# Performance work log

Measured on AMD Instinct MI355X. Metric: run time of the kernel, lower is better.

The kernel has to match this reference:

```python
import jax, jax.numpy as jnp
import numpy as np

VOCAB = 4101
NUM_IGNORED = 5  # token ids {0,1,2,3,4} are ignored


def _calc_frequency(x):
    # x: [N, L] int token ids -> [N, VOCAB] scaled frequency vectors
    n = x.shape[0]
    hist = jnp.zeros((n, VOCAB), dtype=jnp.float32)
    hist = hist.at[jnp.arange(n)[:, None], x].add(1.0)  # batched bincount
    hist = hist.at[:, :NUM_IGNORED].set(0.0)            # drop ignored tokens
    seq_len = hist.sum(axis=-1, keepdims=True)          # count of kept tokens
    return jnp.where(seq_len > 0, hist / seq_len * 10.0, hist)


def _mlp(h, W1, b1, W2, b2):
    h = jax.nn.relu(h @ W1 + b1)
    return h @ W2 + b2


def setup_inputs() -> dict:
    key = jax.random.key(0)
    k1, k2, k3 = jax.random.split(key, 3)
    B, L = 1024, 4096
    X = jax.random.randint(k1, (B, 3, L), 0, VOCAB, dtype=jnp.int64)
    W1 = jax.random.normal(k2, (VOCAB, 768), dtype=jnp.float32) * 0.02
    b1 = jnp.zeros((768,), dtype=jnp.float32)
    W2 = jax.random.normal(k3, (768, 256), dtype=jnp.float32) * 0.02
    b2 = jnp.zeros((256,), dtype=jnp.float32)
    return {"X": X, "W1": W1, "b1": b1, "W2": W2, "b2": b2}


def reference(X, W1, b1, W2, b2):
    B, three, L = X.shape
    flat = X.reshape(B * three, L)          # process anchor/pos/neg together
    freq = _calc_frequency(flat)            # [3B, VOCAB]
    out = _mlp(freq, W1, b1, W2, b2)        # [3B, 256]
    out = out.reshape(B, three, 256)
    return (out[:, 0], out[:, 1], out[:, 2])
```

## Files before the change

kernel.cpp:

```cpp
#include <hip/hip_runtime.h>

typedef unsigned short ushort_t;
typedef __bf16 bf16_8 __attribute__((ext_vector_type(8)));
typedef float f32x4 __attribute__((ext_vector_type(4)));

#define VOCAB 4101
#define KPAD  4224
#define NROWS 3072
#define HDIM  768
#define ODIM  256


static __device__ __forceinline__ unsigned short f2bf(float f) {
  unsigned int u = __float_as_uint(f);
  unsigned int r = (u + 0x7fffu + ((u >> 16) & 1u)) >> 16;
  return (unsigned short)r;
}

static __device__ __forceinline__ void async_copy16(const void* g, void* l) {
  __builtin_amdgcn_global_load_lds(
      (const __attribute__((address_space(1))) void*)g,
      (__attribute__((address_space(3))) void*)l, 16, 0, 0);
}


__global__ __launch_bounds__(256)
void prep_kernel(const int* __restrict__ X,
                 const float* __restrict__ W1,
                 const float* __restrict__ W2,
                 ushort_t* __restrict__ A,
                 ushort_t* __restrict__ W1T,
                 ushort_t* __restrict__ W2T,
                 float* __restrict__ scales) {
  __shared__ __align__(16) unsigned char smem[16896];
  const int bid = blockIdx.x;

  if (bid < NROWS) {
    unsigned int* h = (unsigned int*)smem;
    const int r = bid;
    for (int i = threadIdx.x; i < KPAD; i += 256) h[i] = 0u;
    __syncthreads();

    const int4* xp = reinterpret_cast<const int4*>(X + (size_t)r * 4096);
    #pragma unroll
    for (int i = 0; i < 4; ++i) {
      int4 v = xp[i * 256 + threadIdx.x];
      atomicAdd(&h[v.x], 1u);
      atomicAdd(&h[v.y], 1u);
      atomicAdd(&h[v.z], 1u);
      atomicAdd(&h[v.w], 1u);
    }
    __syncthreads();

    const unsigned int ignored = h[0] + h[1] + h[2] + h[3] + h[4];
    const float s = 10.0f / (float)(4096u - ignored);
    if (threadIdx.x == 0) scales[r] = s;

    unsigned int* Ar = (unsigned int*)(A + (size_t)r * KPAD);
    for (int i = threadIdx.x; i < KPAD / 2; i += 256) {
      int i0 = 2 * i, i1 = 2 * i + 1;
      unsigned int c0 = (i0 >= 5 && i0 < VOCAB) ? h[i0] : 0u;
      unsigned int c1 = (i1 >= 5 && i1 < VOCAB) ? h[i1] : 0u;
      Ar[i] = (unsigned int)f2bf((float)c0) | ((unsigned int)f2bf((float)c1) << 16);
    }
  } else {
    ushort_t (*tile)[65] = (ushort_t(*)[65])smem;
    const float* src; ushort_t* dst;
    int K, N, Kpad, kb, nb;
    if (bid < NROWS + 792) {
      const int t = bid - NROWS;
      src = W1; dst = W1T; K = VOCAB; N = HDIM; Kpad = KPAD;
      kb = (t % 66) * 64; nb = (t / 66) * 64;
    } else {
      const int t = bid - NROWS - 792;
      src = W2; dst = W2T; K = HDIM; N = ODIM; Kpad = HDIM;
      kb = (t % 12) * 64; nb = (t / 12) * 64;
    }
    const int tr = threadIdx.x >> 6;
    const int tc = threadIdx.x & 63;
    #pragma unroll
    for (int i = 0; i < 16; ++i) {
      int r = i * 4 + tr;
      int k = kb + r;
      float v = (k < K) ? src[(size_t)k * N + nb + tc] : 0.0f;
      tile[r][tc] = f2bf(v);
    }
    __syncthreads();
    #pragma unroll
    for (int i = 0; i < 16; ++i) {
      int r = i * 4 + tr;
      dst[(size_t)(nb + r) * Kpad + kb + tc] = tile[tc][r];
    }
  }
}


__global__ __launch_bounds__(256)
void gemm1_fused(const ushort_t* __restrict__ A, int lda,
                 const ushort_t* __restrict__ Bt, int ldb,
                 int ktiles,
                 const float* __restrict__ scales,
                 const float* __restrict__ bias,
                 ushort_t* __restrict__ H) {
  __shared__ __align__(16) ushort_t Alds[2][96 * 128];
  __shared__ __align__(16) ushort_t Blds[2][96 * 128];
  const int tid  = threadIdx.x;
  const int lane = tid & 63;
  const int wv   = tid >> 6;
  const int wrow = wv >> 1;
  const int wcol = wv & 1;
  const int m0   = blockIdx.x * 96;
  const int n0   = blockIdx.y * 96;

  f32x4 acc[3][3];
  #pragma unroll
  for (int m = 0; m < 3; ++m)
    #pragma unroll
    for (int n = 0; n < 3; ++n)
      acc[m][n] = (f32x4){0.f, 0.f, 0.f, 0.f};

#define STAGE(bi, kt)                                                          \
  {                                                                            \
    const int k0_ = (kt) * 128;                                                \
    _Pragma("unroll")                                                          \
    for (int i = 0; i < 6; ++i) {                                              \
      const int cd  = i * 256 + tid;                                           \
      const int row = cd >> 4;                                                 \
      const int cc  = (cd & 15) ^ (row & 7);                                   \
      async_copy16(A + (size_t)(m0 + row) * lda + k0_ + cc * 8,                \
                   (char*)&Alds[bi][0] + cd * 16);                             \
    }                                                                          \
    _Pragma("unroll")                                                          \
    for (int i = 0; i < 6; ++i) {                                              \
      const int cd  = i * 256 + tid;                                           \
      const int row = cd >> 4;                                                 \
      const int cc  = (cd & 15) ^ (row & 7);                                   \
      async_copy16(Bt + (size_t)(n0 + row) * ldb + k0_ + cc * 8,               \
                   (char*)&Blds[bi][0] + cd * 16);                             \
    }                                                                          \
  }

  STAGE(0, 0);
  __syncthreads();

  int cur = 0;
  for (int t = 0; t < ktiles; ++t) {
    if (t + 1 < ktiles) STAGE(cur ^ 1, t + 1);
    const int hi = lane >> 4;
    #pragma unroll
    for (int kk = 0; kk < 4; ++kk) {
      bf16_8 af[3], bf[3];
      #pragma unroll
      for (int m = 0; m < 3; ++m) {
        const int ra = wrow * 48 + m * 16 + (lane & 15);
        const int ca = kk * 4 + hi;
        af[m] = *(const bf16_8*)((const char*)&Alds[cur][0] +
                                 (ra * 16 + (ca ^ (ra & 7))) * 16);
      }
      #pragma unroll
      for (int n = 0; n < 3; ++n) {
        const int rb = wcol * 48 + n * 16 + (lane & 15);
        const int cb = kk * 4 + hi;
        bf[n] = *(const bf16_8*)((const char*)&Blds[cur][0] +
                                 (rb * 16 + (cb ^ (rb & 7))) * 16);
      }
      #pragma unroll
      for (int m = 0; m < 3; ++m)
        #pragma unroll
        for (int n = 0; n < 3; ++n)
          acc[m][n] = __builtin_amdgcn_mfma_f32_16x16x32_bf16(af[m], bf[n],
                                                              acc[m][n], 0, 0, 0);
    }
    __syncthreads();
    cur ^= 1;
  }
#undef STAGE

  const int rbase = (lane >> 4) * 4;
  const int cf    = lane & 15;
  #pragma unroll
  for (int m = 0; m < 3; ++m) {
    #pragma unroll
    for (int n = 0; n < 3; ++n) {
      #pragma unroll
      for (int reg = 0; reg < 4; ++reg) {
        const int gr = m0 + wrow * 48 + m * 16 + rbase + reg;
        const int gc = n0 + wcol * 48 + n * 16 + cf;
        float v = fmaxf(acc[m][n][reg] * scales[gr] + bias[gc], 0.0f);
        H[(size_t)gr * HDIM + gc] = f2bf(v);
      }
    }
  }
}


__global__ __launch_bounds__(384)
void gemm2_fused(const ushort_t* __restrict__ A, int lda,
                 const ushort_t* __restrict__ Bt, int ldb,
                 int ktiles,
                 const float* __restrict__ bias,
                 float* __restrict__ outp) {
  __shared__ __align__(16) ushort_t Alds[2][96 * 128];
  __shared__ __align__(16) ushort_t Blds[2][32 * 128];
  const int tid  = threadIdx.x;
  const int lane = tid & 63;
  const int wv   = tid >> 6;
  const int m0   = blockIdx.x * 96;
  const int n0   = blockIdx.y * 32;

  f32x4 acc[2];
  acc[0] = (f32x4){0.f, 0.f, 0.f, 0.f};
  acc[1] = (f32x4){0.f, 0.f, 0.f, 0.f};

#define STAGE(bi, kt)                                                          \
  {                                                                            \
    const int k0_ = (kt) * 128;                                                \
    _Pragma("unroll")                                                          \
    for (int i = 0; i < 4; ++i) {                                              \
      const int cd  = i * 384 + tid;                                           \
      const int row = cd >> 4;                                                 \
      const int cc  = (cd & 15) ^ (row & 7);                                   \
      async_copy16(A + (size_t)(m0 + row) * lda + k0_ + cc * 8,                \
                   (char*)&Alds[bi][0] + cd * 16);                             \
    }                                                                          \
    {                                                                          \
      const int cd  = tid;                                                     \
      const int row = cd >> 4;                                                 \
      const int cc  = (cd & 15) ^ (row & 7);                                   \
      async_copy16(Bt + (size_t)(n0 + row) * ldb + k0_ + cc * 8,               \
                   (char*)&Blds[bi][0] + cd * 16);                             \
    }                                                                          \
    if (tid < 128) {                                                           \
      const int cd  = 384 + tid;                                               \
      const int row = cd >> 4;                                                 \
      const int cc  = (cd & 15) ^ (row & 7);                                   \
      async_copy16(Bt + (size_t)(n0 + row) * ldb + k0_ + cc * 8,               \
                   (char*)&Blds[bi][0] + cd * 16);                             \
    }                                                                          \
  }

  STAGE(0, 0);
  __syncthreads();

  int cur = 0;
  for (int t = 0; t < ktiles; ++t) {
    if (t + 1 < ktiles) STAGE(cur ^ 1, t + 1);
    const int hi = lane >> 4;
    #pragma unroll
    for (int kk = 0; kk < 4; ++kk) {
      bf16_8 af, bf[2];
      {
        const int ra = wv * 16 + (lane & 15);
        const int ca = kk * 4 + hi;
        af = *(const bf16_8*)((const char*)&Alds[cur][0] +
                              (ra * 16 + (ca ^ (ra & 7))) * 16);
      }
      #pragma unroll
      for (int n = 0; n < 2; ++n) {
        const int rb = n * 16 + (lane & 15);
        const int cb = kk * 4 + hi;
        bf[n] = *(const bf16_8*)((const char*)&Blds[cur][0] +
                                 (rb * 16 + (cb ^ (rb & 7))) * 16);
      }
      #pragma unroll
      for (int n = 0; n < 2; ++n)
        acc[n] = __builtin_amdgcn_mfma_f32_16x16x32_bf16(af, bf[n], acc[n], 0, 0, 0);
    }
    __syncthreads();
    cur ^= 1;
  }
#undef STAGE

  const int rbase = (lane >> 4) * 4;
  const int cf    = lane & 15;
  #pragma unroll
  for (int n = 0; n < 2; ++n) {
    #pragma unroll
    for (int reg = 0; reg < 4; ++reg) {
      const int gr = m0 + wv * 16 + rbase + reg;
      const int gc = n0 + n * 16 + cf;
      float v = acc[n][reg] + bias[gc];
      outp[(size_t)(gr % 3) * (1024 * ODIM) + (size_t)(gr / 3) * ODIM + gc] = v;
    }
  }
}


extern "C" void kernel_launch(void* const* d_in, const int* in_sizes, int n_in,
                              void* d_out, int out_size, void* d_ws, size_t ws_size,
                              hipStream_t stream) {
  const int*   X  = (const int*)d_in[0];
  const float* W1 = (const float*)d_in[1];
  const float* b1 = (const float*)d_in[2];
  const float* W2 = (const float*)d_in[3];
  const float* b2 = (const float*)d_in[4];
  float* out = (float*)d_out;

  char* ws = (char*)d_ws;
  ushort_t* A      = (ushort_t*)(ws);
  ushort_t* W1T    = (ushort_t*)(ws + 25952256);
  ushort_t* H      = (ushort_t*)(ws + 32440320);
  ushort_t* W2T    = (ushort_t*)(ws + 37158912);
  float*    scales = (float*)   (ws + 37552128);

  prep_kernel<<<NROWS + 792 + 48, 256, 0, stream>>>(X, W1, W2, A, W1T, W2T, scales);

  gemm1_fused<<<dim3(NROWS / 96, HDIM / 96), 256, 0, stream>>>(
      A, KPAD, W1T, KPAD, KPAD / 128, scales, b1, H);

  gemm2_fused<<<dim3(NROWS / 96, ODIM / 32), 384, 0, stream>>>(
      H, HDIM, W2T, HDIM, HDIM / 128, b2, out);
}
```

Measured before the change: 63.16 us.

## Shrink gemm1 tile to 96x48 with two waves and vectorize histogram stores

The first GEMM now uses 96x48 output tiles with 128 threads (two waves, each owning 48 rows), which doubles the grid to 512 blocks so more CUs are busy on a 256-CU part. The cost is more redundant A-tile loading per output, since each A tile is reused across only 48 columns. Separately, the prep kernel zeroes the histogram and writes the bf16 frequency row with 16-byte vector stores instead of 4-byte ones, cutting the number of store instructions.

```diff
diff --git a/kernel.cpp b/kernel.cpp
--- a/kernel.cpp
+++ b/kernel.cpp
@@ -38,7 +38,9 @@
   if (bid < NROWS) {
     unsigned int* h = (unsigned int*)smem;
     const int r = bid;
-    for (int i = threadIdx.x; i < KPAD; i += 256) h[i] = 0u;
+    uint4* h4 = (uint4*)smem;
+    for (int i = threadIdx.x; i < 1056; i += 256)
+      h4[i] = (uint4){0u, 0u, 0u, 0u};
     __syncthreads();
 
     const int4* xp = reinterpret_cast<const int4*>(X + (size_t)r * 4096);
@@ -56,12 +58,18 @@
     const float s = 10.0f / (float)(4096u - ignored);
     if (threadIdx.x == 0) scales[r] = s;
 
-    unsigned int* Ar = (unsigned int*)(A + (size_t)r * KPAD);
-    for (int i = threadIdx.x; i < KPAD / 2; i += 256) {
-      int i0 = 2 * i, i1 = 2 * i + 1;
-      unsigned int c0 = (i0 >= 5 && i0 < VOCAB) ? h[i0] : 0u;
-      unsigned int c1 = (i1 >= 5 && i1 < VOCAB) ? h[i1] : 0u;
-      Ar[i] = (unsigned int)f2bf((float)c0) | ((unsigned int)f2bf((float)c1) << 16);
+    uint4* Ar4 = (uint4*)(A + (size_t)r * KPAD);
+    for (int i = threadIdx.x; i < 528; i += 256) {
+      const int b0 = i * 8;
+      unsigned int w[4];
+      #pragma unroll
+      for (int j = 0; j < 4; ++j) {
+        int ia = b0 + 2 * j, ib = b0 + 2 * j + 1;
+        unsigned int ca = (ia >= 5 && ia < VOCAB) ? h[ia] : 0u;
+        unsigned int cb = (ib >= 5 && ib < VOCAB) ? h[ib] : 0u;
+        w[j] = (unsigned int)f2bf((float)ca) | ((unsigned int)f2bf((float)cb) << 16);
+      }
+      Ar4[i] = (uint4){w[0], w[1], w[2], w[3]};
     }
   } else {
     ushort_t (*tile)[65] = (ushort_t(*)[65])smem;
@@ -95,7 +103,7 @@
 }
 
 
-__global__ __launch_bounds__(256)
+__global__ __launch_bounds__(128)
 void gemm1_fused(const ushort_t* __restrict__ A, int lda,
                  const ushort_t* __restrict__ Bt, int ldb,
                  int ktiles,
@@ -103,14 +111,12 @@
                  const float* __restrict__ bias,
                  ushort_t* __restrict__ H) {
   __shared__ __align__(16) ushort_t Alds[2][96 * 128];
-  __shared__ __align__(16) ushort_t Blds[2][96 * 128];
+  __shared__ __align__(16) ushort_t Blds[2][48 * 128];
   const int tid  = threadIdx.x;
   const int lane = tid & 63;
   const int wv   = tid >> 6;
-  const int wrow = wv >> 1;
-  const int wcol = wv & 1;
   const int m0   = blockIdx.x * 96;
-  const int n0   = blockIdx.y * 96;
+  const int n0   = blockIdx.y * 48;
 
   f32x4 acc[3][3];
   #pragma unroll
@@ -123,8 +129,8 @@
   {                                                                            \
     const int k0_ = (kt) * 128;                                                \
     _Pragma("unroll")                                                          \
-    for (int i = 0; i < 6; ++i) {                                              \
-      const int cd  = i * 256 + tid;                                           \
+    for (int i = 0; i < 12; ++i) {                                             \
+      const int cd  = i * 128 + tid;                                           \
       const int row = cd >> 4;                                                 \
       const int cc  = (cd & 15) ^ (row & 7);                                   \
       async_copy16(A + (size_t)(m0 + row) * lda + k0_ + cc * 8,                \
@@ -132,7 +138,7 @@
     }                                                                          \
     _Pragma("unroll")                                                          \
     for (int i = 0; i < 6; ++i) {                                              \
-      const int cd  = i * 256 + tid;                                           \
+      const int cd  = i * 128 + tid;                                           \
       const int row = cd >> 4;                                                 \
       const int cc  = (cd & 15) ^ (row & 7);                                   \
       async_copy16(Bt + (size_t)(n0 + row) * ldb + k0_ + cc * 8,               \
@@ -152,14 +158,14 @@
       bf16_8 af[3], bf[3];
       #pragma unroll
       for (int m = 0; m < 3; ++m) {
-        const int ra = wrow * 48 + m * 16 + (lane & 15);
+        const int ra = wv * 48 + m * 16 + (lane & 15);
         const int ca = kk * 4 + hi;
         af[m] = *(const bf16_8*)((const char*)&Alds[cur][0] +
                                  (ra * 16 + (ca ^ (ra & 7))) * 16);
       }
       #pragma unroll
       for (int n = 0; n < 3; ++n) {
-        const int rb = wcol * 48 + n * 16 + (lane & 15);
+        const int rb = n * 16 + (lane & 15);
         const int cb = kk * 4 + hi;
         bf[n] = *(const bf16_8*)((const char*)&Blds[cur][0] +
                                  (rb * 16 + (cb ^ (rb & 7))) * 16);
@@ -184,8 +190,8 @@
     for (int n = 0; n < 3; ++n) {
       #pragma unroll
       for (int reg = 0; reg < 4; ++reg) {
-        const int gr = m0 + wrow * 48 + m * 16 + rbase + reg;
-        const int gc = n0 + wcol * 48 + n * 16 + cf;
+        const int gr = m0 + wv * 48 + m * 16 + rbase + reg;
+        const int gc = n0 + n * 16 + cf;
         float v = fmaxf(acc[m][n][reg] * scales[gr] + bias[gc], 0.0f);
         H[(size_t)gr * HDIM + gc] = f2bf(v);
       }
@@ -305,7 +311,7 @@
 
   prep_kernel<<<NROWS + 792 + 48, 256, 0, stream>>>(X, W1, W2, A, W1T, W2T, scales);
 
-  gemm1_fused<<<dim3(NROWS / 96, HDIM / 96), 256, 0, stream>>>(
+  gemm1_fused<<<dim3(NROWS / 96, HDIM / 48), 128, 0, stream>>>(
       A, KPAD, W1T, KPAD, KPAD / 128, scales, b1, H);
 
   gemm2_fused<<<dim3(NROWS / 96, ODIM / 32), 384, 0, stream>>>(
```

Result: slower. 67.35 us (+6.6%).
